# Kernel optimization log

Hardware: AMD Instinct MI355X
Metric: run time of the kernel (lower is better)

The kernel has to match this reference:

```python
import jax, jax.numpy as jnp
import numpy as np

B, N, CIN, H, COUT = 256, 400, 128, 128, 16
THRESH = 0.6
EPS = 1e-5


def setup_inputs() -> dict:
    key = jax.random.key(0)
    ks = jax.random.split(key, 20)
    rn = lambda k, s, sc: jax.random.normal(k, s, jnp.float32) * sc
    inp = {
        "x": rn(ks[0], (B, N, CIN), 1.0),
        "adj": rn(ks[1], (B, N, N), 1.0),
        "edge": jax.random.randint(ks[2], (2, 4096), 0, N),  # unused (recomputed from adj in original)
        "batch": jnp.repeat(jnp.arange(B), N).reshape(B, N),  # graph ids; dense layout => mean over axis 1
        "W_adj": rn(ks[3], (N, N), 1.0 / np.sqrt(N)),
        "b_adj": rn(ks[4], (N,), 0.02),
        "W1": rn(ks[5], (CIN, H), 1.0 / np.sqrt(CIN)),
        "a_src1": rn(ks[6], (H,), 1.0 / np.sqrt(H)),
        "a_dst1": rn(ks[7], (H,), 1.0 / np.sqrt(H)),
        "b1": rn(ks[8], (H,), 0.02),
        "W2": rn(ks[9], (H, H), 1.0 / np.sqrt(H)),
        "a_src2": rn(ks[10], (H,), 1.0 / np.sqrt(H)),
        "a_dst2": rn(ks[11], (H,), 1.0 / np.sqrt(H)),
        "b2": rn(ks[12], (H,), 0.02),
        "ln_g": jnp.ones((H,), jnp.float32),
        "ln_b": jnp.zeros((H,), jnp.float32),
        "W_lin": rn(ks[13], (H, COUT), 1.0 / np.sqrt(H)),
        "b_lin": rn(ks[14], (COUT,), 0.02),
    }
    return inp


def _layer_norm(x, g, b):
    m = x.mean(-1, keepdims=True)
    v = ((x - m) ** 2).mean(-1, keepdims=True)
    return (x - m) * jax.lax.rsqrt(v + EPS) * g + b


def _gat(h, mask, W, a_src, a_dst, b):
    # PyG GATConv (1 head): edge i(src)->j(dst), softmax over incoming src nodes.
    hp = h @ W                                   # [B,N,H]
    e_src = hp @ a_src                           # [B,N]
    e_dst = hp @ a_dst                           # [B,N]
    score = jax.nn.leaky_relu(e_src[:, :, None] + e_dst[:, None, :], 0.2)  # [B,S,D]
    score = jnp.where(mask, score, jnp.finfo(score.dtype).min)
    alpha = jax.nn.softmax(score, axis=1)        # softmax over source axis per dst
    return jnp.einsum('bsd,bsh->bdh', alpha, hp) + b


def reference(x, adj, edge, batch, W_adj, b_adj, W1, a_src1, a_dst1, b1,
              W2, a_src2, a_dst2, b2, ln_g, ln_b, W_lin, b_lin):
    # adj -> Linear -> sigmoid -> detach -> threshold(0.6) -> binary edge mask
    a = jax.nn.sigmoid(adj @ W_adj + b_adj)
    mask = jax.lax.stop_gradient(a > THRESH)
    mask = mask | jnp.eye(N, dtype=bool)         # GATConv add_self_loops=True

    h = _gat(x, mask, W1, a_src1, a_dst1, b1)
    h = jax.nn.relu(_layer_norm(h, ln_g, ln_b))
    h = _gat(h, mask, W2, a_src2, a_dst2, b2)
    h = jax.nn.relu(_layer_norm(h, ln_g, ln_b))
    h = _gat(h, mask, W2, a_src2, a_dst2, b2)    # conv2 applied twice in original
    g = h.mean(axis=1)                           # global_mean_pool (dense per-graph layout)
    # dropout p=0.5 is identity in eval mode
    return g @ W_lin + b_lin                     # [B, COUT]
```

## Files before the change

### kernel.cpp

```cpp
#include <hip/hip_runtime.h>
#include <hip/hip_bf16.h>
#include <math.h>

#define NB 256
#define NN 400
#define NH 128
#define NCOUT 16
#define NNP 416
#define KP  416

static constexpr float LOGIT_THRESH = 0.40546510810816444f;
static constexpr float LN_EPS = 1e-5f;

typedef __attribute__((ext_vector_type(8))) short short8v;
typedef __attribute__((ext_vector_type(4))) float f32x4;

static __device__ __forceinline__ short f2bf_rne(float f) {
    unsigned u = __float_as_uint(f);
    unsigned r = (u + 0x7fff + ((u >> 16) & 1)) >> 16;
    return (short)r;
}
static __device__ __forceinline__ float bf2f(short s) {
    return __uint_as_float(((unsigned)(unsigned short)s) << 16);
}

static __device__ __forceinline__ unsigned pk_bf16(float a, float b) {
    __hip_bfloat162 h = __float22bfloat162_rn(make_float2(a, b));
    unsigned r;
    __builtin_memcpy(&r, &h, 4);
    return r;
}
static __device__ __forceinline__ void cvt8v(const float x[8], short8v& hv) {
    unsigned* hp = (unsigned*)&hv;
#pragma unroll
    for (int q = 0; q < 4; ++q) hp[q] = pk_bf16(x[2 * q], x[2 * q + 1]);
}

static __device__ __forceinline__ void gload16(const void* g, void* l) {
    __builtin_amdgcn_global_load_lds((const __attribute__((address_space(1))) void*)g,
                                     (__attribute__((address_space(3))) void*)l, 16, 0, 0);
}

__global__ __launch_bounds__(256) void k_wprep(const float* __restrict__ W,
                                               short* __restrict__ WtH)
{
    const int k0 = blockIdx.x * 32, d0 = blockIdx.y * 32;
    __shared__ float tile[32][33];
    const int t = threadIdx.x, cc = t & 31, rr = t >> 5;
#pragma unroll
    for (int i = 0; i < 4; ++i) {
        int k = k0 + rr + i * 8, d = d0 + cc;
        tile[rr + i * 8][cc] = (k < NN && d < NN) ? W[k * NN + d] : 0.f;
    }
    __syncthreads();
#pragma unroll
    for (int i = 0; i < 4; ++i) {
        int dr = rr + i * 8;
        int d = d0 + dr, k = k0 + cc;
        WtH[d * KP + k] = f2bf_rne(tile[cc][dr]);
    }
}

__global__ __launch_bounds__(256) void k_wprepW(const float* __restrict__ W,
                                                short* __restrict__ WTH)
{
    const int t = blockIdx.x * 256 + threadIdx.x;
    const int h = t >> 7, k = t & 127;
    WTH[h * NH + k] = f2bf_rne(W[k * NH + h]);
}

__global__ __launch_bounds__(256) void k_mask(const float* __restrict__ adj,
                                              const short* __restrict__ WtH,
                                              const float* __restrict__ badj,
                                              unsigned char* __restrict__ maskT)
{
    const int j   = blockIdx.x;
    const int xcd = j & 7;
    const int li  = j >> 3;
    const int panel  = xcd * 128 + (li >> 2);
    const int member = li & 3;
    const int b  = panel >> 2;
    const int s0 = (panel & 3) * 128;
    const int d0 = member * 128;

    const int t = threadIdx.x;
    const int lane = t & 63, w = t >> 6;
    const int wm = w >> 1, wn = w & 1;
    const int fr = lane & 15, fc = lane >> 4;

    __shared__ float As[2][128 * 32];
    __shared__ short Bhs[2][128 * 32];

    const float* adjb = adj + (long)b * NN * NN;

    long aG[4];
    int  aRow[4];
#pragma unroll
    for (int i = 0; i < 4; ++i) {
        int rloc = w * 32 + i * 8 + (lane >> 3);
        aRow[i] = rloc;
        int srow = s0 + rloc; srow = srow < NN ? srow : NN - 1;
        int c = (lane & 7) ^ (rloc & 7);
        aG[i] = (long)srow * NN + c * 4;
    }
    long bG[2];
#pragma unroll
    for (int i = 0; i < 2; ++i) {
        int rloc = w * 32 + i * 16 + (lane >> 2);
        int drow = d0 + rloc;
        int c = (lane & 3) ^ ((rloc >> 1) & 3);
        bG[i] = (long)drow * KP + c * 8;
    }

    f32x4 acc[4][4];
#pragma unroll
    for (int mi = 0; mi < 4; ++mi)
#pragma unroll
        for (int ni = 0; ni < 4; ++ni) acc[mi][ni] = (f32x4){0.f, 0.f, 0.f, 0.f};

    const int ca0 = (2 * fc) ^ (fr & 7);
    const int ca1 = (2 * fc + 1) ^ (fr & 7);
    const int cb  = fc ^ ((fr >> 1) & 3);

    #define STAGE(KT, BUF)                                                            \
    do {                                                                              \
        const int k0_ = (KT) * 32;                                                    \
        _Pragma("unroll")                                                             \
        for (int i = 0; i < 4; ++i) {                                                 \
            long gi = aG[i] + k0_;                                                    \
            if ((KT) == 12) {                                                         \
                int c = (lane & 7) ^ (aRow[i] & 7);                                   \
                if (c >= 4) gi = aG[i] - (long)c * 4;                                 \
            }                                                                         \
            gload16(adjb + gi, (char*)&As[BUF][0] + (w * 32 + i * 8) * 128);          \
        }                                                                             \
        _Pragma("unroll")                                                             \
        for (int i = 0; i < 2; ++i) {                                                 \
            gload16(WtH + bG[i] + k0_, (char*)&Bhs[BUF][0] + (w * 32 + i * 16) * 64); \
        }                                                                             \
    } while (0)

    STAGE(0, 0);
    asm volatile("s_waitcnt vmcnt(0)" ::: "memory");
    __builtin_amdgcn_s_barrier();

    int cur = 0;
    for (int kt = 0; kt < 13; ++kt) {
        __builtin_amdgcn_s_barrier();
        if (kt < 12) STAGE(kt + 1, cur ^ 1);
        if (kt < 12) asm volatile("s_waitcnt vmcnt(6)" ::: "memory");
        else         asm volatile("s_waitcnt vmcnt(0)" ::: "memory");
        __builtin_amdgcn_s_barrier();
        __builtin_amdgcn_sched_barrier(0);

        short8v ah[4], bh[4];
#pragma unroll
        for (int m = 0; m < 4; ++m) {
            const int row = wm * 64 + m * 16 + fr;
            float4 u0 = *(const float4*)((const char*)&As[cur][0] + row * 128 + ca0 * 16);
            float4 u1 = *(const float4*)((const char*)&As[cur][0] + row * 128 + ca1 * 16);
            float x[8] = {u0.x, u0.y, u0.z, u0.w, u1.x, u1.y, u1.z, u1.w};
            cvt8v(x, ah[m]);
        }
#pragma unroll
        for (int n = 0; n < 4; ++n) {
            const int row = wn * 64 + n * 16 + fr;
            bh[n] = *(const short8v*)((const char*)&Bhs[cur][0] + row * 64 + cb * 16);
        }
#pragma unroll
        for (int mi = 0; mi < 4; ++mi)
#pragma unroll
            for (int ni = 0; ni < 4; ++ni)
                acc[mi][ni] = __builtin_amdgcn_mfma_f32_16x16x32_bf16(ah[mi], bh[ni], acc[mi][ni], 0, 0, 0);
        cur ^= 1;
    }
    #undef STAGE

    unsigned char* mTb = maskT + (long)b * 32 * 52 * 128;
    const int dgbase = (d0 >> 4) + wn * 4;
    const int scbase = ((s0 + wm * 64) >> 3) + (fc >> 1);
    const int off8   = (fc & 1) * 4;
#pragma unroll
    for (int ni = 0; ni < 4; ++ni) {
        const int d = d0 + wn * 64 + ni * 16 + fr;
        if (d >= NN) continue;
        const float bv = badj[d];
#pragma unroll
        for (int mi = 0; mi < 4; ++mi) {
            const int s_cb = s0 + wm * 64 + mi * 16 + fc * 4;
            if (s_cb >= NNP) continue;
            uchar4 pk;
#pragma unroll
            for (int jj = 0; jj < 4; ++jj) {
                const int s = s_cb + jj;
                bool v = (s < NN) && ((acc[mi][ni][jj] + bv) > LOGIT_THRESH || s == d);
                ((unsigned char*)&pk)[jj] = v ? 1 : 0;
            }
            *(uchar4*)&mTb[((long)(dgbase + ni) * 52 + (scbase + mi * 2)) * 128 + fr * 8 + off8] = pk;
        }
    }
}

__global__ __launch_bounds__(256) void k_hp(const float* __restrict__ hin,
                                            const short* __restrict__ WTH,
                                            const float* __restrict__ asrc,
                                            const float* __restrict__ adst,
                                            short* __restrict__ hpT,
                                            float* __restrict__ e1sA, float* __restrict__ e2sA,
                                            float* __restrict__ e1dA, float* __restrict__ e2dA)
{
    const int b  = blockIdx.y;
    const int s0 = blockIdx.x * 128;
    const int t  = threadIdx.x;
    const int lane = t & 63, w = t >> 6;
    const int wm = w >> 1, wn = w & 1;
    const int fr = lane & 15, fc = lane >> 4;

    const float* hb = hin + (long)b * NN * NH;
    short* hpTb = hpT + (long)b * 52 * 128 * 8;

    f32x4 acc[4][4];
#pragma unroll
    for (int m = 0; m < 4; ++m)
#pragma unroll
        for (int n = 0; n < 4; ++n) acc[m][n] = (f32x4){0.f, 0.f, 0.f, 0.f};

    for (int kt = 0; kt < 4; ++kt) {
        const int k0 = kt * 32;
        short8v ah[4], bh[4];
#pragma unroll
        for (int m = 0; m < 4; ++m) {
            const int h = wm * 64 + m * 16 + fr;
            ah[m] = *(const short8v*)&WTH[h * NH + k0 + fc * 8];
        }
#pragma unroll
        for (int n = 0; n < 4; ++n) {
            const int s = s0 + wn * 64 + n * 16 + fr;
            float x[8];
            if (s < NN) {
                float4 u0 = *(const float4*)&hb[(long)s * NH + k0 + fc * 8];
                float4 u1 = *(const float4*)&hb[(long)s * NH + k0 + fc * 8 + 4];
                x[0]=u0.x; x[1]=u0.y; x[2]=u0.z; x[3]=u0.w;
                x[4]=u1.x; x[5]=u1.y; x[6]=u1.z; x[7]=u1.w;
            } else {
#pragma unroll
                for (int jj = 0; jj < 8; ++jj) x[jj] = 0.f;
            }
            cvt8v(x, bh[n]);
        }
#pragma unroll
        for (int m = 0; m < 4; ++m)
#pragma unroll
            for (int n = 0; n < 4; ++n)
                acc[m][n] = __builtin_amdgcn_mfma_f32_16x16x32_bf16(ah[m], bh[n], acc[m][n], 0, 0, 0);
    }

#pragma unroll
    for (int m = 0; m < 4; ++m) {
#pragma unroll
        for (int n = 0; n < 4; ++n) {
            const int s = s0 + wn * 64 + n * 16 + fr;
            if (s >= NNP) continue;
            const int sc = s >> 3, so = s & 7;
#pragma unroll
            for (int jj = 0; jj < 4; ++jj) {
                const int h = wm * 64 + m * 16 + fc * 4 + jj;
                hpTb[((long)sc * 128 + h) * 8 + so] = f2bf_rne(acc[m][n][jj]);
            }
        }
    }

    __shared__ float esp[2][128], edp[2][128];
    float asv[4][4], adv[4][4];
#pragma unroll
    for (int m = 0; m < 4; ++m)
#pragma unroll
        for (int jj = 0; jj < 4; ++jj) {
            const int h = wm * 64 + m * 16 + fc * 4 + jj;
            asv[m][jj] = asrc[h];
            adv[m][jj] = adst[h];
        }
    float ps[4] = {0.f, 0.f, 0.f, 0.f}, pd[4] = {0.f, 0.f, 0.f, 0.f};
#pragma unroll
    for (int n = 0; n < 4; ++n)
#pragma unroll
        for (int m = 0; m < 4; ++m)
#pragma unroll
            for (int jj = 0; jj < 4; ++jj) {
                ps[n] += acc[m][n][jj] * asv[m][jj];
                pd[n] += acc[m][n][jj] * adv[m][jj];
            }
#pragma unroll
    for (int n = 0; n < 4; ++n) {
        ps[n] += __shfl_xor(ps[n], 16); ps[n] += __shfl_xor(ps[n], 32);
        pd[n] += __shfl_xor(pd[n], 16); pd[n] += __shfl_xor(pd[n], 32);
    }
    if (fc == 0) {
#pragma unroll
        for (int n = 0; n < 4; ++n) {
            esp[wm][wn * 64 + n * 16 + fr] = ps[n];
            edp[wm][wn * 64 + n * 16 + fr] = pd[n];
        }
    }
    __syncthreads();
    if (t < 128) {
        const int s = s0 + t;
        if (s < NNP) {
            const float es = esp[0][t] + esp[1][t];
            const float ed = edp[0][t] + edp[1][t];
            const long o = (long)b * NNP + s;
            e1sA[o] = __expf(es);       e2sA[o] = __expf(0.2f * es);
            e1dA[o] = __expf(ed);       e2dA[o] = __expf(0.2f * ed);
        }
    }
}

template<int DO_LN>
__global__ __launch_bounds__(256) void k_aggr(const unsigned char* __restrict__ maskT,
                                              const short* __restrict__ hpT,
                                              const float* __restrict__ e1sA,
                                              const float* __restrict__ e2sA,
                                              const float* __restrict__ e1dA,
                                              const float* __restrict__ e2dA,
                                              const float* __restrict__ bias,
                                              const float* __restrict__ lng,
                                              const float* __restrict__ lnb,
                                              float* __restrict__ hout,
                                              float* __restrict__ partial)
{
    const int b  = blockIdx.y;
    const int bx = blockIdx.x;
    const int d0 = bx * 128;
    const int t  = threadIdx.x;
    const int lane = t & 63, w = t >> 6;
    const int fr = lane & 15, fc = lane >> 4;

    __shared__ float e1s_l[NNP], e2s_l[NNP];
    __shared__ float den_l[128];
    __shared__ float lngl[128], lnbl[128];
    __shared__ float wsum[4][128];

    for (int i = t; i < NNP; i += 256) {
        const long o = (long)b * NNP + i;
        e1s_l[i] = e1sA[o];
        e2s_l[i] = e2sA[o];
    }
    if (DO_LN && t < 128) { lngl[t] = lng[t]; lnbl[t] = lnb[t]; }

    float e1dv[2], e2dv[2];
#pragma unroll
    for (int m = 0; m < 2; ++m) {
        const int d = d0 + w * 32 + m * 16 + fr;
        const bool v = d < NN;
        const long o = (long)b * NNP + (v ? d : 0);
        e1dv[m] = v ? e1dA[o] : 0.f;
        e2dv[m] = v ? e2dA[o] : 0.f;
    }
    __syncthreads();

    f32x4 acc[2][8];
#pragma unroll
    for (int m = 0; m < 2; ++m)
#pragma unroll
        for (int n = 0; n < 8; ++n) acc[m][n] = (f32x4){0.f, 0.f, 0.f, 0.f};
    float den[2] = {0.f, 0.f};

    const unsigned char* mbase = maskT + (((long)b * 32 + (d0 >> 4) + w * 2) * 52) * 128 + fr * 8;
    const short* hTb = hpT + (long)b * 52 * 128 * 8;

    for (int kt = 0; kt < 13; ++kt) {
        const int sb = kt * 32 + fc * 8;
        const short* tb = hTb + (long)(kt * 4 + fc) * 128 * 8;
        short8v bf_[8];
#pragma unroll
        for (int n = 0; n < 8; ++n)
            bf_[n] = *(const short8v*)&tb[(n * 16 + fr) * 8];
        float4 e1a = *(const float4*)&e1s_l[sb];
        float4 e1b = *(const float4*)&e1s_l[sb + 4];
        float4 e2a = *(const float4*)&e2s_l[sb];
        float4 e2b = *(const float4*)&e2s_l[sb + 4];
        float e18[8] = {e1a.x, e1a.y, e1a.z, e1a.w, e1b.x, e1b.y, e1b.z, e1b.w};
        float e28[8] = {e2a.x, e2a.y, e2a.z, e2a.w, e2b.x, e2b.y, e2b.z, e2b.w};
        const long scoff = (long)(kt * 4 + fc) * 128;
#pragma unroll
        for (int m = 0; m < 2; ++m) {
            const unsigned long long mk = *(const unsigned long long*)(mbase + (long)m * 52 * 128 + scoff);
            short8v pv;
            unsigned* pw = (unsigned*)&pv;
#pragma unroll
            for (int q = 0; q < 4; ++q) {
                float p0 = fmaxf(e18[2 * q] * e1dv[m],     e28[2 * q] * e2dv[m]);
                float p1 = fmaxf(e18[2 * q + 1] * e1dv[m], e28[2 * q + 1] * e2dv[m]);
                p0 = ((mk >> (16 * q)) & 0xffULL)     ? p0 : 0.f;
                p1 = ((mk >> (16 * q + 8)) & 0xffULL) ? p1 : 0.f;
                den[m] += p0 + p1;
                pw[q] = pk_bf16(p0, p1);
            }
#pragma unroll
            for (int n = 0; n < 8; ++n)
                acc[m][n] = __builtin_amdgcn_mfma_f32_16x16x32_bf16(pv, bf_[n], acc[m][n], 0, 0, 0);
        }
    }

#pragma unroll
    for (int m = 0; m < 2; ++m) {
        den[m] += __shfl_xor(den[m], 16);
        den[m] += __shfl_xor(den[m], 32);
    }
    if (fc == 0) {
#pragma unroll
        for (int m = 0; m < 2; ++m) den_l[w * 32 + m * 16 + fr] = den[m];
    }
    __syncthreads();

    float bvh[8], lgv[8], lbv[8];
#pragma unroll
    for (int n = 0; n < 8; ++n) {
        bvh[n] = bias[n * 16 + fr];
        if (DO_LN) { lgv[n] = lngl[n * 16 + fr]; lbv[n] = lnbl[n * 16 + fr]; }
    }

    float* hb = hout + (long)b * NN * NH;

    if (DO_LN) {
#pragma unroll
        for (int m = 0; m < 2; ++m) {
#pragma unroll
            for (int jj = 0; jj < 4; ++jj) {
                const int dl = w * 32 + m * 16 + fc * 4 + jj;
                const int d = d0 + dl;
                const float idn = 1.f / den_l[dl];
                float v[8];
                float s1 = 0.f, s2 = 0.f;
#pragma unroll
                for (int n = 0; n < 8; ++n) {
                    v[n] = acc[m][n][jj] * idn + bvh[n];
                    s1 += v[n];
                    s2 += v[n] * v[n];
                }
                s1 += __shfl_xor(s1, 1); s2 += __shfl_xor(s2, 1);
                s1 += __shfl_xor(s1, 2); s2 += __shfl_xor(s2, 2);
                s1 += __shfl_xor(s1, 4); s2 += __shfl_xor(s2, 4);
                s1 += __shfl_xor(s1, 8); s2 += __shfl_xor(s2, 8);
                const float mean = s1 * (1.f / 128.f);
                const float var  = s2 * (1.f / 128.f) - mean * mean;
                const float inv  = rsqrtf(fmaxf(var, 0.f) + LN_EPS);
                if (d < NN) {
                    float* po = hb + (long)d * NH;
#pragma unroll
                    for (int n = 0; n < 8; ++n)
                        po[n * 16 + fr] = fmaxf((v[n] - mean) * inv * lgv[n] + lbv[n], 0.f);
                }
            }
        }
    } else {
        float psum[8] = {0.f, 0.f, 0.f, 0.f, 0.f, 0.f, 0.f, 0.f};
#pragma unroll
        for (int m = 0; m < 2; ++m) {
#pragma unroll
            for (int jj = 0; jj < 4; ++jj) {
                const int dl = w * 32 + m * 16 + fc * 4 + jj;
                const int d = d0 + dl;
                if (d >= NN) continue;
                const float idn = 1.f / den_l[dl];
#pragma unroll
                for (int n = 0; n < 8; ++n)
                    psum[n] += acc[m][n][jj] * idn + bvh[n];
            }
        }
#pragma unroll
        for (int n = 0; n < 8; ++n) {
            psum[n] += __shfl_xor(psum[n], 16);
            psum[n] += __shfl_xor(psum[n], 32);
        }
        if (fc == 0) {
#pragma unroll
            for (int n = 0; n < 8; ++n) wsum[w][n * 16 + fr] = psum[n];
        }
        __syncthreads();
        if (t < 128)
            partial[((long)b * 4 + bx) * 128 + t] =
                wsum[0][t] + wsum[1][t] + wsum[2][t] + wsum[3][t];
    }
}

__global__ __launch_bounds__(128) void k_pool2(const float* __restrict__ partial,
                                               const float* __restrict__ Wl,
                                               const float* __restrict__ bl,
                                               float* __restrict__ out)
{
    const int b = blockIdx.x;
    const int t = threadIdx.x;
    const float* pb = partial + (long)b * 4 * 128;
    __shared__ float gl[128];
    gl[t] = (pb[t] + pb[128 + t] + pb[256 + t] + pb[384 + t]) * (1.f / NN);
    __syncthreads();
    if (t < NCOUT) {
        float o = bl[t];
        for (int k = 0; k < NH; ++k) o += gl[k] * Wl[k * NCOUT + t];
        out[b * NCOUT + t] = o;
    }
}

extern "C" void kernel_launch(void* const* d_in, const int* in_sizes, int n_in,
                              void* d_out, int out_size, void* d_ws, size_t ws_size,
                              hipStream_t stream)
{
    const float* x    = (const float*)d_in[0];
    const float* adj  = (const float*)d_in[1];
    const float* Wadj = (const float*)d_in[4];
    const float* badj = (const float*)d_in[5];
    const float* W1   = (const float*)d_in[6];
    const float* as1  = (const float*)d_in[7];
    const float* ad1  = (const float*)d_in[8];
    const float* b1   = (const float*)d_in[9];
    const float* W2   = (const float*)d_in[10];
    const float* as2  = (const float*)d_in[11];
    const float* ad2  = (const float*)d_in[12];
    const float* b2   = (const float*)d_in[13];
    const float* lng  = (const float*)d_in[14];
    const float* lnb  = (const float*)d_in[15];
    const float* Wlin = (const float*)d_in[16];
    const float* blin = (const float*)d_in[17];
    float* out = (float*)d_out;

    char* ws = (char*)d_ws;
    unsigned char* maskT = (unsigned char*)ws;
    short* hpT  = (short*)(ws + 54525952);
    float* hbuf = (float*)(ws + 81788928);
    float* e1sA = (float*)(ws + 134217728);
    float* e2sA = (float*)(ws + 134643712);
    float* e1dA = (float*)(ws + 135069696);
    float* e2dA = (float*)(ws + 135495680);
    short* WtH  = (short*)(ws + 135921664);
    short* WT1H = (short*)(ws + 136347648);
    short* WT2H = (short*)(ws + 136380416);
    float* partial = (float*)(ws + 136413184);

    k_wprep<<<dim3(13, 16), dim3(256), 0, stream>>>(Wadj, WtH);
    k_wprepW<<<dim3(64), dim3(256), 0, stream>>>(W1, WT1H);
    k_wprepW<<<dim3(64), dim3(256), 0, stream>>>(W2, WT2H);
    k_mask<<<dim3(4096), dim3(256), 0, stream>>>(adj, WtH, badj, maskT);

    k_hp<<<dim3(4, NB), dim3(256), 0, stream>>>(x, WT1H, as1, ad1, hpT,
                                                e1sA, e2sA, e1dA, e2dA);
    k_aggr<1><<<dim3(4, NB), dim3(256), 0, stream>>>(maskT, hpT, e1sA, e2sA, e1dA, e2dA,
                                                     b1, lng, lnb, hbuf, partial);

    k_hp<<<dim3(4, NB), dim3(256), 0, stream>>>(hbuf, WT2H, as2, ad2, hpT,
                                                e1sA, e2sA, e1dA, e2dA);
    k_aggr<1><<<dim3(4, NB), dim3(256), 0, stream>>>(maskT, hpT, e1sA, e2sA, e1dA, e2dA,
                                                     b2, lng, lnb, hbuf, partial);

    k_hp<<<dim3(4, NB), dim3(256), 0, stream>>>(hbuf, WT2H, as2, ad2, hpT,
                                                e1sA, e2sA, e1dA, e2dA);
    k_aggr<0><<<dim3(4, NB), dim3(256), 0, stream>>>(maskT, hpT, e1sA, e2sA, e1dA, e2dA,
                                                     b2, lng, lnb, hbuf, partial);

    k_pool2<<<dim3(NB), dim3(128), 0, stream>>>(partial, Wlin, blin, out);
}
```

Measured before the change: 357.6 us.

## Stage mask GEMM through registers with bf16 LDS tiles instead of direct-to-LDS loads

The adj-mask GEMM kernel used to copy fp32 adj tiles straight into LDS with global_load_lds and convert them to bf16 after every LDS read. It now loads each tile into registers two steps ahead, converts it to bf16 once, and writes bf16 tiles into a swizzled double buffer. This halves LDS usage for A and removes the repeated conversion work, and an occupancy hint of 4 blocks per CU is added. In exchange it needs more registers to hold the in-flight tiles, and the extra register-to-LDS write step could lengthen each iteration.

```diff
diff --git a/kernel.cpp b/kernel.cpp
--- a/kernel.cpp
+++ b/kernel.cpp
@@ -20,9 +20,6 @@
     unsigned r = (u + 0x7fff + ((u >> 16) & 1)) >> 16;
     return (short)r;
 }
-static __device__ __forceinline__ float bf2f(short s) {
-    return __uint_as_float(((unsigned)(unsigned short)s) << 16);
-}
 
 static __device__ __forceinline__ unsigned pk_bf16(float a, float b) {
     __hip_bfloat162 h = __float22bfloat162_rn(make_float2(a, b));
@@ -36,11 +33,6 @@
     for (int q = 0; q < 4; ++q) hp[q] = pk_bf16(x[2 * q], x[2 * q + 1]);
 }
 
-static __device__ __forceinline__ void gload16(const void* g, void* l) {
-    __builtin_amdgcn_global_load_lds((const __attribute__((address_space(1))) void*)g,
-                                     (__attribute__((address_space(3))) void*)l, 16, 0, 0);
-}
-
 __global__ __launch_bounds__(256) void k_wprep(const float* __restrict__ W,
                                                short* __restrict__ WtH)
 {
@@ -69,10 +61,10 @@
     WTH[h * NH + k] = f2bf_rne(W[k * NH + h]);
 }
 
-__global__ __launch_bounds__(256) void k_mask(const float* __restrict__ adj,
-                                              const short* __restrict__ WtH,
-                                              const float* __restrict__ badj,
-                                              unsigned char* __restrict__ maskT)
+__global__ __launch_bounds__(256, 4) void k_mask(const float* __restrict__ adj,
+                                                 const short* __restrict__ WtH,
+                                                 const float* __restrict__ badj,
+                                                 unsigned char* __restrict__ maskT)
 {
     const int j   = blockIdx.x;
     const int xcd = j & 7;
@@ -88,29 +80,24 @@
     const int wm = w >> 1, wn = w & 1;
     const int fr = lane & 15, fc = lane >> 4;
 
-    __shared__ float As[2][128 * 32];
-    __shared__ short Bhs[2][128 * 32];
+    __shared__ short Abf[2][128 * 32];
+    __shared__ short Bbf[2][128 * 32];
 
     const float* adjb = adj + (long)b * NN * NN;
 
-    long aG[4];
-    int  aRow[4];
-#pragma unroll
-    for (int i = 0; i < 4; ++i) {
-        int rloc = w * 32 + i * 8 + (lane >> 3);
-        aRow[i] = rloc;
-        int srow = s0 + rloc; srow = srow < NN ? srow : NN - 1;
-        int c = (lane & 7) ^ (rloc & 7);
-        aG[i] = (long)srow * NN + c * 4;
-    }
-    long bG[2];
-#pragma unroll
-    for (int i = 0; i < 2; ++i) {
-        int rloc = w * 32 + i * 16 + (lane >> 2);
-        int drow = d0 + rloc;
-        int c = (lane & 3) ^ ((rloc >> 1) & 3);
-        bG[i] = (long)drow * KP + c * 8;
-    }
+    const int ra  = t >> 1;
+    const int ch2 = t & 1;
+    int sra = s0 + ra; sra = sra < NN ? sra : NN - 1;
+    const float* aSrc = adjb + (long)sra * NN + ch2 * 16;
+    const short* bSrc = WtH + (long)(d0 + ra) * KP + ch2 * 16;
+
+    const int aswz = (ra >> 1) & 3;
+    const int ac0 = (ch2 * 2) ^ aswz;
+    const int ac1 = (ch2 * 2 + 1) ^ aswz;
+    short* aD0[2] = { &Abf[0][ra * 32 + ac0 * 8], &Abf[1][ra * 32 + ac0 * 8] };
+    short* aD1[2] = { &Abf[0][ra * 32 + ac1 * 8], &Abf[1][ra * 32 + ac1 * 8] };
+    short* bD0[2] = { &Bbf[0][ra * 32 + ac0 * 8], &Bbf[1][ra * 32 + ac0 * 8] };
+    short* bD1[2] = { &Bbf[0][ra * 32 + ac1 * 8], &Bbf[1][ra * 32 + ac1 * 8] };
 
     f32x4 acc[4][4];
 #pragma unroll
@@ -118,63 +105,63 @@
 #pragma unroll
         for (int ni = 0; ni < 4; ++ni) acc[mi][ni] = (f32x4){0.f, 0.f, 0.f, 0.f};
 
-    const int ca0 = (2 * fc) ^ (fr & 7);
-    const int ca1 = (2 * fc + 1) ^ (fr & 7);
-    const int cb  = fc ^ ((fr >> 1) & 3);
-
-    #define STAGE(KT, BUF)                                                            \
-    do {                                                                              \
-        const int k0_ = (KT) * 32;                                                    \
-        _Pragma("unroll")                                                             \
-        for (int i = 0; i < 4; ++i) {                                                 \
-            long gi = aG[i] + k0_;                                                    \
-            if ((KT) == 12) {                                                         \
-                int c = (lane & 7) ^ (aRow[i] & 7);                                   \
-                if (c >= 4) gi = aG[i] - (long)c * 4;                                 \
-            }                                                                         \
-            gload16(adjb + gi, (char*)&As[BUF][0] + (w * 32 + i * 8) * 128);          \
-        }                                                                             \
-        _Pragma("unroll")                                                             \
-        for (int i = 0; i < 2; ++i) {                                                 \
-            gload16(WtH + bG[i] + k0_, (char*)&Bhs[BUF][0] + (w * 32 + i * 16) * 64); \
-        }                                                                             \
+    float4 a0, a1, a2, a3;
+    short8v bv0, bv1;
+
+    #define LOADT(KT)                                                       \
+    do {                                                                    \
+        if ((KT) == 12 && ch2 == 1) {                                       \
+            a0 = a1 = a2 = a3 = make_float4(0.f, 0.f, 0.f, 0.f);            \
+        } else {                                                            \
+            const float* p_ = aSrc + (KT) * 32;                             \
+            a0 = *(const float4*)(p_);     a1 = *(const float4*)(p_ + 4);   \
+            a2 = *(const float4*)(p_ + 8); a3 = *(const float4*)(p_ + 12);  \
+        }                                                                   \
+        const short* q_ = bSrc + (KT) * 32;                                 \
+        bv0 = *(const short8v*)(q_);                                        \
+        bv1 = *(const short8v*)(q_ + 8);                                    \
     } while (0)
 
-    STAGE(0, 0);
-    asm volatile("s_waitcnt vmcnt(0)" ::: "memory");
-    __builtin_amdgcn_s_barrier();
-
+    #define WRITET(BUF)                                                     \
+    do {                                                                    \
+        short8v h0, h1;                                                     \
+        float xa[8] = {a0.x, a0.y, a0.z, a0.w, a1.x, a1.y, a1.z, a1.w};     \
+        float xb[8] = {a2.x, a2.y, a2.z, a2.w, a3.x, a3.y, a3.z, a3.w};     \
+        cvt8v(xa, h0); cvt8v(xb, h1);                                       \
+        *(short8v*)aD0[BUF] = h0;                                           \
+        *(short8v*)aD1[BUF] = h1;                                           \
+        *(short8v*)bD0[BUF] = bv0;                                          \
+        *(short8v*)bD1[BUF] = bv1;                                          \
+    } while (0)
+
+    LOADT(0);
+    WRITET(0);
+    __syncthreads();
+    LOADT(1);
+
+    const int cbr = fc ^ ((fr >> 1) & 3);
     int cur = 0;
     for (int kt = 0; kt < 13; ++kt) {
-        __builtin_amdgcn_s_barrier();
-        if (kt < 12) STAGE(kt + 1, cur ^ 1);
-        if (kt < 12) asm volatile("s_waitcnt vmcnt(6)" ::: "memory");
-        else         asm volatile("s_waitcnt vmcnt(0)" ::: "memory");
-        __builtin_amdgcn_s_barrier();
-        __builtin_amdgcn_sched_barrier(0);
-
         short8v ah[4], bh[4];
 #pragma unroll
-        for (int m = 0; m < 4; ++m) {
-            const int row = wm * 64 + m * 16 + fr;
-            float4 u0 = *(const float4*)((const char*)&As[cur][0] + row * 128 + ca0 * 16);
-            float4 u1 = *(const float4*)((const char*)&As[cur][0] + row * 128 + ca1 * 16);
-            float x[8] = {u0.x, u0.y, u0.z, u0.w, u1.x, u1.y, u1.z, u1.w};
-            cvt8v(x, ah[m]);
-        }
-#pragma unroll
-        for (int n = 0; n < 4; ++n) {
-            const int row = wn * 64 + n * 16 + fr;
-            bh[n] = *(const short8v*)((const char*)&Bhs[cur][0] + row * 64 + cb * 16);
-        }
+        for (int m = 0; m < 4; ++m)
+            ah[m] = *(const short8v*)&Abf[cur][(wm * 64 + m * 16 + fr) * 32 + cbr * 8];
+#pragma unroll
+        for (int n = 0; n < 4; ++n)
+            bh[n] = *(const short8v*)&Bbf[cur][(wn * 64 + n * 16 + fr) * 32 + cbr * 8];
 #pragma unroll
         for (int mi = 0; mi < 4; ++mi)
 #pragma unroll
             for (int ni = 0; ni < 4; ++ni)
                 acc[mi][ni] = __builtin_amdgcn_mfma_f32_16x16x32_bf16(ah[mi], bh[ni], acc[mi][ni], 0, 0, 0);
+
+        if (kt < 12) WRITET(cur ^ 1);
+        if (kt < 11) LOADT(kt + 2);
+        __syncthreads();
         cur ^= 1;
     }
-    #undef STAGE
+    #undef LOADT
+    #undef WRITET
 
     unsigned char* mTb = maskT + (long)b * 32 * 52 * 128;
     const int dgbase = (d0 >> 4) + wn * 4;
```

Measured after the change: 370.7 us. 1.04x slower.
